# Performance work log

Hardware: AMD Instinct MI355X
Metric: run time of the kernel (lower is better)

The kernel has to match this reference:

```python
import jax, jax.numpy as jnp
import numpy as np

VOCAB = 128000
EMB = 32          # emb_dim
HALF = EMB // 2   # embedding table width
B, S = 1024, 50
PAD, UNK = 0, 1


def setup_inputs() -> dict:
    key = jax.random.key(0)
    ks = jax.random.split(key, 9)
    text = jax.random.randint(ks[0], (B, S), 0, VOCAB)
    emb_weight = jax.random.normal(ks[1], (VOCAB, HALF), jnp.float32) * 0.02
    emb_weight = emb_weight.at[PAD].set(0.0)  # padding_idx zeroed
    fc0_w = jax.random.normal(ks[2], (EMB, HALF), jnp.float32) * 0.1
    fc0_b = jax.random.normal(ks[3], (EMB,), jnp.float32) * 0.01
    att_wq = jax.random.normal(ks[4], (EMB, EMB), jnp.float32) * 0.1
    att_wk = jax.random.normal(ks[5], (EMB, EMB), jnp.float32) * 0.1
    att_v = jax.random.normal(ks[6], (EMB,), jnp.float32) * 0.1
    out_w = jax.random.normal(ks[7], (EMB, 2 * EMB), jnp.float32) * 0.1
    out_b = jax.random.normal(ks[8], (EMB,), jnp.float32) * 0.01
    return {
        "text": text, "emb_weight": emb_weight,
        "fc0_w": fc0_w, "fc0_b": fc0_b,
        "att_wq": att_wq, "att_wk": att_wk, "att_v": att_v,
        "out_w": out_w, "out_b": out_b,
    }


def reference(text, emb_weight, fc0_w, fc0_b, att_wq, att_wk, att_v, out_w, out_b):
    # mask: token is neither pad nor unk -> [B,S,1]
    valid = (text != PAD) & (text != UNK)
    mask = valid.astype(jnp.float32)[..., None]
    # embedded = fc0(emb(text)) * mask -> [B,S,EMB]
    embedded = (emb_weight[text] @ fc0_w.T + fc0_b) * mask
    # additive (Bahdanau) attention pooling: score_t = v^T tanh(Wq q_t + Wk k_t)
    scores = jnp.tanh(embedded @ att_wq.T + embedded @ att_wk.T) @ att_v  # [B,S]
    scores = jnp.where(valid, scores, jnp.float32(-1e9))
    attn = jax.nn.softmax(scores, axis=-1)                                # [B,S]
    sg = jnp.einsum("bs,bse->be", attn, embedded)                         # [B,EMB]
    sl = embedded[:, -1, :]                                               # [B,EMB]
    hidden = jnp.concatenate([sg, sl], axis=-1) @ out_w.T + out_b         # [B,EMB]
    # full-vocab head: hidden @ fc0(emb.weight).T -> [B,VOCAB]
    item_vecs = emb_weight @ fc0_w.T + fc0_b                              # [V,EMB]
    return hidden @ item_vecs.T
```

## Files before the change

kernel.cpp:

```cpp
#include <hip/hip_runtime.h>
#include <hip/hip_bf16.h>
#include <math.h>

#define VOCAB 128000
#define EMB   32
#define HALF  16
#define BB    1024
#define SS    50

__global__ __launch_bounds__(256) void k_hidden(
    const int*   __restrict__ text,
    const float* __restrict__ emb_weight,
    const float* __restrict__ fc0_w, const float* __restrict__ fc0_b,
    const float* __restrict__ att_wq, const float* __restrict__ att_wk,
    const float* __restrict__ att_v,
    const float* __restrict__ out_w, const float* __restrict__ out_b,
    float* __restrict__ hiddenT)
{
    __shared__ float s_fc0w[EMB * HALF];
    __shared__ float s_fc0b[EMB];
    __shared__ float s_W[EMB * EMB];
    __shared__ float s_av[EMB];
    __shared__ float s_owT[2 * EMB][EMB];
    __shared__ float s_ob[EMB];

    const int tid = threadIdx.x;
    for (int i = tid; i < EMB * HALF; i += 256) s_fc0w[i] = fc0_w[i];
    for (int i = tid; i < EMB; i += 256) {
        s_fc0b[i] = fc0_b[i];
        s_av[i]   = att_v[i];
        s_ob[i]   = out_b[i];
    }
    for (int i = tid; i < EMB * EMB; i += 256) s_W[i] = att_wq[i] + att_wk[i];
    for (int i = tid; i < 2 * EMB * EMB; i += 256) {
        int e2 = i / (2 * EMB), j = i % (2 * EMB);
        s_owT[j][e2] = out_w[i];
    }
    __syncthreads();

    const int wave = tid >> 6;
    const int lane = tid & 63;
    const int b    = blockIdx.x * 4 + wave;

    const bool has   = (lane < SS);
    const int  t     = has ? text[b * SS + lane] : 0;
    const bool valid = has && (t != 0) && (t != 1);
    const float m    = valid ? 1.0f : 0.0f;

    const float4* erow = (const float4*)(emb_weight + (size_t)t * HALF);
    float4 q0 = erow[0], q1 = erow[1], q2 = erow[2], q3 = erow[3];
    float er[HALF] = {q0.x, q0.y, q0.z, q0.w, q1.x, q1.y, q1.z, q1.w,
                      q2.x, q2.y, q2.z, q2.w, q3.x, q3.y, q3.z, q3.w};

    float emb[EMB];
#pragma unroll
    for (int e = 0; e < EMB; e++) {
        float acc = s_fc0b[e];
#pragma unroll
        for (int h = 0; h < HALF; h++) acc += er[h] * s_fc0w[e * HALF + h];
        emb[e] = acc * m;
    }

    float sc = 0.0f;
#pragma unroll
    for (int j = 0; j < EMB; j++) {
        float acc = 0.0f;
#pragma unroll
        for (int e = 0; e < EMB; e++) acc += emb[e] * s_W[j * EMB + e];
        sc += tanhf(acc) * s_av[j];
    }
    sc = valid ? sc : -1e9f;
    if (!has) sc = -INFINITY;

    float mx = sc;
#pragma unroll
    for (int off = 32; off >= 1; off >>= 1) mx = fmaxf(mx, __shfl_xor(mx, off));
    float ex = __expf(sc - mx);
    ex = expf(sc - mx);
    float sum = ex;
#pragma unroll
    for (int off = 32; off >= 1; off >>= 1) sum += __shfl_xor(sum, off);
    const float attn = ex / sum;

    float slv[EMB];
#pragma unroll
    for (int e = 0; e < EMB; e++) slv[e] = __shfl(emb[e], 49);

#pragma unroll
    for (int e = 0; e < EMB; e++) emb[e] *= attn;
#pragma unroll
    for (int off = 32; off >= 1; off >>= 1) {
#pragma unroll
        for (int e = 0; e < EMB; e++) emb[e] += __shfl_xor(emb[e], off);
    }

    if (lane < EMB) {
        float h = s_ob[lane];
#pragma unroll
        for (int j = 0; j < EMB; j++) h += emb[j] * s_owT[j][lane];
#pragma unroll
        for (int j = 0; j < EMB; j++) h += slv[j] * s_owT[EMB + j][lane];
        hiddenT[lane * BB + b] = h;
    }
}

__global__ __launch_bounds__(256) void k_items(
    const float* __restrict__ emb_weight,
    const float* __restrict__ fc0_w, const float* __restrict__ fc0_b,
    float* __restrict__ ivT)
{
    __shared__ float s_fc0w[EMB * HALF];
    __shared__ float s_fc0b[EMB];
    const int tid = threadIdx.x;
    for (int i = tid; i < EMB * HALF; i += 256) s_fc0w[i] = fc0_w[i];
    for (int i = tid; i < EMB; i += 256) s_fc0b[i] = fc0_b[i];
    __syncthreads();

    const int v = blockIdx.x * 256 + tid;
    const float4* erow = (const float4*)(emb_weight + (size_t)v * HALF);
    float4 q0 = erow[0], q1 = erow[1], q2 = erow[2], q3 = erow[3];
    float er[HALF] = {q0.x, q0.y, q0.z, q0.w, q1.x, q1.y, q1.z, q1.w,
                      q2.x, q2.y, q2.z, q2.w, q3.x, q3.y, q3.z, q3.w};
#pragma unroll
    for (int k = 0; k < EMB; k++) {
        float acc = s_fc0b[k];
#pragma unroll
        for (int h = 0; h < HALF; h++) acc += er[h] * s_fc0w[k * HALF + h];
        ivT[k * VOCAB + v] = acc;
    }
}

__global__ __launch_bounds__(256, 2) void k_out(
    const float* __restrict__ ivT,
    const float* __restrict__ hiddenT,
    float* __restrict__ out)
{
    const int XB = 25, YB = 32;
    const int id    = blockIdx.x;
    const int chunk = id / (XB * YB);
    const int r     = id % (XB * YB);
    const int xb    = chunk * XB + (r % XB);
    const int b0    = (r / XB) * 32;

    const int vq = xb * 256 + threadIdx.x;

    float4 acc[32];
#pragma unroll
    for (int j = 0; j < 32; j++) acc[j] = make_float4(0.f, 0.f, 0.f, 0.f);

    const float4* iv4 = (const float4*)ivT;
#pragma unroll 4
    for (int k = 0; k < EMB; k++) {
        const float4 iv = iv4[k * (VOCAB / 4) + vq];
        const float* hr = hiddenT + k * BB + b0;
#pragma unroll
        for (int j = 0; j < 32; j++) {
            const float h = hr[j];
            acc[j].x += iv.x * h;
            acc[j].y += iv.y * h;
            acc[j].z += iv.z * h;
            acc[j].w += iv.w * h;
        }
    }

    float4* o4 = (float4*)out;
#pragma unroll
    for (int j = 0; j < 32; j++) {
        o4[(b0 + j) * (VOCAB / 4) + vq] = acc[j];
    }
}

extern "C" void kernel_launch(void* const* d_in, const int* in_sizes, int n_in,
                              void* d_out, int out_size, void* d_ws, size_t ws_size,
                              hipStream_t stream) {
    const int*   text       = (const int*)  d_in[0];
    const float* emb_weight = (const float*)d_in[1];
    const float* fc0_w      = (const float*)d_in[2];
    const float* fc0_b      = (const float*)d_in[3];
    const float* att_wq     = (const float*)d_in[4];
    const float* att_wk     = (const float*)d_in[5];
    const float* att_v      = (const float*)d_in[6];
    const float* out_w      = (const float*)d_in[7];
    const float* out_b      = (const float*)d_in[8];
    float* out = (float*)d_out;

    float* ivT     = (float*)d_ws;
    float* hiddenT = (float*)((char*)d_ws + (size_t)EMB * VOCAB * sizeof(float));

    k_items<<<VOCAB / 256, 256, 0, stream>>>(emb_weight, fc0_w, fc0_b, ivT);
    k_hidden<<<BB / 4, 256, 0, stream>>>(text, emb_weight, fc0_w, fc0_b,
                                         att_wq, att_wk, att_v, out_w, out_b, hiddenT);
    k_out<<<4000, 256, 0, stream>>>(ivT, hiddenT, out);
}
```

Measured before the change: 600.6 us.

## Merge prep kernels, shrink output tile, use nontemporal stores for logits

Merges the item-vector and hidden-state kernels into one launch, with block index deciding which work a block does. The output GEMM tile drops from 32 to 16 batch rows per block, doubling the grid and raising the occupancy hint to 4. The large logits output is written with nontemporal stores. The aim is to cut launch overhead, raise occupancy to hide latency, and keep the write-once 512MB output from polluting cache, at the cost of reading the item vectors twice as often.

```diff
diff --git a/kernel.cpp b/kernel.cpp
--- a/kernel.cpp
+++ b/kernel.cpp
@@ -1,5 +1,4 @@
 #include <hip/hip_runtime.h>
-#include <hip/hip_bf16.h>
 #include <math.h>
 
 #define VOCAB 128000
@@ -8,14 +7,16 @@
 #define BB    1024
 #define SS    50
 
-__global__ __launch_bounds__(256) void k_hidden(
+typedef float vfloat4 __attribute__((ext_vector_type(4)));
+
+__global__ __launch_bounds__(256) void k_prep(
     const int*   __restrict__ text,
     const float* __restrict__ emb_weight,
     const float* __restrict__ fc0_w, const float* __restrict__ fc0_b,
     const float* __restrict__ att_wq, const float* __restrict__ att_wk,
     const float* __restrict__ att_v,
     const float* __restrict__ out_w, const float* __restrict__ out_b,
-    float* __restrict__ hiddenT)
+    float* __restrict__ ivT, float* __restrict__ hiddenT)
 {
     __shared__ float s_fc0w[EMB * HALF];
     __shared__ float s_fc0b[EMB];
@@ -25,6 +26,28 @@
     __shared__ float s_ob[EMB];
 
     const int tid = threadIdx.x;
+    const int bid = blockIdx.x;
+
+    if (bid < VOCAB / 256) {
+        for (int i = tid; i < EMB * HALF; i += 256) s_fc0w[i] = fc0_w[i];
+        for (int i = tid; i < EMB; i += 256) s_fc0b[i] = fc0_b[i];
+        __syncthreads();
+
+        const int v = bid * 256 + tid;
+        const float4* erow = (const float4*)(emb_weight + (size_t)v * HALF);
+        float4 q0 = erow[0], q1 = erow[1], q2 = erow[2], q3 = erow[3];
+        float er[HALF] = {q0.x, q0.y, q0.z, q0.w, q1.x, q1.y, q1.z, q1.w,
+                          q2.x, q2.y, q2.z, q2.w, q3.x, q3.y, q3.z, q3.w};
+#pragma unroll
+        for (int k = 0; k < EMB; k++) {
+            float acc = s_fc0b[k];
+#pragma unroll
+            for (int h = 0; h < HALF; h++) acc += er[h] * s_fc0w[k * HALF + h];
+            ivT[k * VOCAB + v] = acc;
+        }
+        return;
+    }
+
     for (int i = tid; i < EMB * HALF; i += 256) s_fc0w[i] = fc0_w[i];
     for (int i = tid; i < EMB; i += 256) {
         s_fc0b[i] = fc0_b[i];
@@ -40,7 +63,7 @@
 
     const int wave = tid >> 6;
     const int lane = tid & 63;
-    const int b    = blockIdx.x * 4 + wave;
+    const int b    = (bid - VOCAB / 256) * 4 + wave;
 
     const bool has   = (lane < SS);
     const int  t     = has ? text[b * SS + lane] : 0;
@@ -75,8 +98,7 @@
     float mx = sc;
 #pragma unroll
     for (int off = 32; off >= 1; off >>= 1) mx = fmaxf(mx, __shfl_xor(mx, off));
-    float ex = __expf(sc - mx);
-    ex = expf(sc - mx);
+    float ex = expf(sc - mx);
     float sum = ex;
 #pragma unroll
     for (int off = 32; off >= 1; off >>= 1) sum += __shfl_xor(sum, off);
@@ -104,57 +126,31 @@
     }
 }
 
-__global__ __launch_bounds__(256) void k_items(
-    const float* __restrict__ emb_weight,
-    const float* __restrict__ fc0_w, const float* __restrict__ fc0_b,
-    float* __restrict__ ivT)
-{
-    __shared__ float s_fc0w[EMB * HALF];
-    __shared__ float s_fc0b[EMB];
-    const int tid = threadIdx.x;
-    for (int i = tid; i < EMB * HALF; i += 256) s_fc0w[i] = fc0_w[i];
-    for (int i = tid; i < EMB; i += 256) s_fc0b[i] = fc0_b[i];
-    __syncthreads();
-
-    const int v = blockIdx.x * 256 + tid;
-    const float4* erow = (const float4*)(emb_weight + (size_t)v * HALF);
-    float4 q0 = erow[0], q1 = erow[1], q2 = erow[2], q3 = erow[3];
-    float er[HALF] = {q0.x, q0.y, q0.z, q0.w, q1.x, q1.y, q1.z, q1.w,
-                      q2.x, q2.y, q2.z, q2.w, q3.x, q3.y, q3.z, q3.w};
-#pragma unroll
-    for (int k = 0; k < EMB; k++) {
-        float acc = s_fc0b[k];
-#pragma unroll
-        for (int h = 0; h < HALF; h++) acc += er[h] * s_fc0w[k * HALF + h];
-        ivT[k * VOCAB + v] = acc;
-    }
-}
-
-__global__ __launch_bounds__(256, 2) void k_out(
+__global__ __launch_bounds__(256, 4) void k_out(
     const float* __restrict__ ivT,
     const float* __restrict__ hiddenT,
     float* __restrict__ out)
 {
-    const int XB = 25, YB = 32;
+    const int XB = 25, YB = 64;
     const int id    = blockIdx.x;
     const int chunk = id / (XB * YB);
     const int r     = id % (XB * YB);
     const int xb    = chunk * XB + (r % XB);
-    const int b0    = (r / XB) * 32;
+    const int b0    = (r / XB) * 16;
 
     const int vq = xb * 256 + threadIdx.x;
 
-    float4 acc[32];
+    float4 acc[16];
 #pragma unroll
-    for (int j = 0; j < 32; j++) acc[j] = make_float4(0.f, 0.f, 0.f, 0.f);
+    for (int j = 0; j < 16; j++) acc[j] = make_float4(0.f, 0.f, 0.f, 0.f);
 
     const float4* iv4 = (const float4*)ivT;
-#pragma unroll 4
+#pragma unroll 8
     for (int k = 0; k < EMB; k++) {
         const float4 iv = iv4[k * (VOCAB / 4) + vq];
         const float* hr = hiddenT + k * BB + b0;
 #pragma unroll
-        for (int j = 0; j < 32; j++) {
+        for (int j = 0; j < 16; j++) {
             const float h = hr[j];
             acc[j].x += iv.x * h;
             acc[j].y += iv.y * h;
@@ -163,10 +159,12 @@
         }
     }
 
-    float4* o4 = (float4*)out;
+    vfloat4* o4 = (vfloat4*)out;
 #pragma unroll
-    for (int j = 0; j < 32; j++) {
-        o4[(b0 + j) * (VOCAB / 4) + vq] = acc[j];
+    for (int j = 0; j < 16; j++) {
+        vfloat4 s;
+        s.x = acc[j].x; s.y = acc[j].y; s.z = acc[j].z; s.w = acc[j].w;
+        __builtin_nontemporal_store(s, &o4[(b0 + j) * (VOCAB / 4) + vq]);
     }
 }
 
@@ -187,8 +185,8 @@
     float* ivT     = (float*)d_ws;
     float* hiddenT = (float*)((char*)d_ws + (size_t)EMB * VOCAB * sizeof(float));
 
-    k_items<<<VOCAB / 256, 256, 0, stream>>>(emb_weight, fc0_w, fc0_b, ivT);
-    k_hidden<<<BB / 4, 256, 0, stream>>>(text, emb_weight, fc0_w, fc0_b,
-                                         att_wq, att_wk, att_v, out_w, out_b, hiddenT);
-    k_out<<<4000, 256, 0, stream>>>(ivT, hiddenT, out);
+    k_prep<<<VOCAB / 256 + BB / 4, 256, 0, stream>>>(
+        text, emb_weight, fc0_w, fc0_b, att_wq, att_wk, att_v, out_w, out_b,
+        ivT, hiddenT);
+    k_out<<<8000, 256, 0, stream>>>(ivT, hiddenT, out);
 }
```

New measurement: 586.6 us. 2.3% less time.
